# Kernel tuning notes

Hardware: AMD Instinct MI355X
Metric: run time of the kernel (lower is better)

## Reference

```python
import jax, jax.numpy as jnp
import numpy as np

N, E, F_IN, EDGE_DIM, H, C, NUM_RELS = 20000, 160000, 64, 8, 4, 128, 4


def setup_inputs() -> dict:
    key = jax.random.key(0)
    ks = jax.random.split(key, 20)
    def rn(k, shape, s=0.05):
        return jax.random.normal(k, shape, jnp.float32) * s
    return {
        "x": rn(ks[0], (N, F_IN), 1.0),
        "edge_index": jax.random.randint(ks[1], (2, E), 0, N, dtype=jnp.int32),
        "edge_features": rn(ks[2], (E, EDGE_DIM), 1.0),
        "W1": rn(ks[3], (F_IN, H * C)), "a_src1": rn(ks[4], (H, C)), "a_dst1": rn(ks[5], (H, C)),
        "We1": rn(ks[6], (EDGE_DIM, H * C)), "a_e1": rn(ks[7], (H, C)), "b1": jnp.zeros((H * C,), jnp.float32),
        "W2": rn(ks[8], (H * C, H * C)), "a_src2": rn(ks[9], (H, C)), "a_dst2": rn(ks[10], (H, C)),
        "We2": rn(ks[11], (EDGE_DIM, H * C)), "a_e2": rn(ks[12], (H, C)), "b2": jnp.zeros((H * C,), jnp.float32),
        "Wd1": rn(ks[13], (2 * H * C, 256)), "bd1": jnp.zeros((256,), jnp.float32),
        "Wd2": rn(ks[14], (256, NUM_RELS)), "bd2": jnp.zeros((NUM_RELS,), jnp.float32),
    }


def _add_self_loops(ei, ea, n):
    # PyG add_self_loops with fill_value='mean': self-loop edge_attr is the
    # mean of incoming edge_attr per destination node (0 if no incoming edges).
    dst = ei[1]
    s = jax.ops.segment_sum(ea, dst, num_segments=n)
    cnt = jax.ops.segment_sum(jnp.ones((ea.shape[0], 1), ea.dtype), dst, num_segments=n)
    mean = s / jnp.maximum(cnt, 1.0)
    loop = jnp.arange(n, dtype=ei.dtype)
    ei2 = jnp.concatenate([ei, jnp.stack([loop, loop])], axis=1)
    ea2 = jnp.concatenate([ea, mean], axis=0)
    return ei2, ea2


def _gat_conv(x, ei, ea, W, a_s, a_d, We, a_e, b, n):
    ei, ea = _add_self_loops(ei, ea, n)
    src, dst = ei[0], ei[1]
    xp = (x @ W).reshape(n, H, C)                      # [N,H,C]
    alpha_s = jnp.einsum('nhc,hc->nh', xp, a_s)        # [N,H]
    alpha_d = jnp.einsum('nhc,hc->nh', xp, a_d)        # [N,H]
    ep = (ea @ We).reshape(-1, H, C)                   # [E',H,C]
    alpha_e = jnp.einsum('ehc,hc->eh', ep, a_e)        # [E',H]
    alpha = alpha_s[src] + alpha_d[dst] + alpha_e
    alpha = jax.nn.leaky_relu(alpha, 0.2)
    # segment softmax over edges sharing a destination node
    m = jax.ops.segment_max(alpha, dst, num_segments=n)
    ex = jnp.exp(alpha - m[dst])
    den = jax.ops.segment_sum(ex, dst, num_segments=n)
    w = ex / den[dst]                                   # [E',H]
    out = jax.ops.segment_sum(xp[src] * w[..., None], dst, num_segments=n)  # [N,H,C]
    return out.reshape(n, H * C) + b


def reference(x, edge_index, edge_features, W1, a_src1, a_dst1, We1, a_e1, b1,
              W2, a_src2, a_dst2, We2, a_e2, b2, Wd1, bd1, Wd2, bd2):
    n = x.shape[0]
    z = jax.nn.elu(_gat_conv(x, edge_index, edge_features, W1, a_src1, a_dst1, We1, a_e1, b1, n))
    z = jax.nn.elu(_gat_conv(z, edge_index, edge_features, W2, a_src2, a_dst2, We2, a_e2, b2, n))
    src, dst = edge_index[0], edge_index[1]
    rel = jnp.concatenate([z[src], z[dst]], axis=1)     # [E, 2*512]
    h = rel @ Wd1 + bd1                                 # dropout is identity at inference
    return jax.nn.sigmoid(h @ Wd2 + bd2)
```

## Files before the change

kernel.cpp:

```cpp
#include <hip/hip_runtime.h>
#include <hip/hip_bf16.h>
#include <math.h>

#define N_NODES 20000
#define N_EDGES 160000
#define FIN 64
#define EDGE_DIM 8
#define H_HEADS 4
#define C_CH 128
#define HC 512
#define NUM_RELS 4
#define E_TOT (N_EDGES + N_NODES)
#define E_PAD 320256

typedef __bf16 bf16x8 __attribute__((ext_vector_type(8)));
typedef __bf16 bf16x4 __attribute__((ext_vector_type(4)));
typedef float f32x4 __attribute__((ext_vector_type(4)));
typedef unsigned short u16x8 __attribute__((ext_vector_type(8)));

#define NZ4 ((N_NODES + E_PAD) / 4)
#define NM4 (E_PAD / 4)
__global__ void k_fill(int4* __restrict__ zbase, int4* __restrict__ mbase) {
    int tid = blockIdx.x * 256 + threadIdx.x;
    if (tid < NZ4) {
        zbase[tid] = make_int4(0, 0, 0, 0);
    } else if (tid < NZ4 + NM4) {
        mbase[tid - NZ4] = make_int4(-1, -1, -1, -1);
    }
}

#define NX4 (N_NODES * FIN / 4)
#define W1T (HC * FIN)
#define W2T (HC * HC)
#define NCVTB ((NX4 + W1T + W2T) / 256)
__global__ void k_prep_all(const float* __restrict__ x, __bf16* __restrict__ xb,
                           const float* __restrict__ W1, __bf16* __restrict__ Wt1,
                           const float* __restrict__ W2, __bf16* __restrict__ Wt2,
                           const float* __restrict__ We1, const float* __restrict__ ae1,
                           const float* __restrict__ We2, const float* __restrict__ ae2,
                           float* __restrict__ q1, float* __restrict__ q2,
                           const float* __restrict__ Wd1, const float* __restrict__ Wd2,
                           const float* __restrict__ bd1, const float* __restrict__ bd2,
                           float* __restrict__ M, float* __restrict__ cvec,
                           const float* __restrict__ as1, const float* __restrict__ ad1,
                           float* __restrict__ w1as, float* __restrict__ w1ad) {
    int bid = blockIdx.x;
    if (bid < NCVTB) {
        int tid = bid * 256 + threadIdx.x;
        if (tid < NX4) {
            float4 v = *(const float4*)(x + (size_t)tid * 4);
            __bf16 o[4] = {(__bf16)v.x, (__bf16)v.y, (__bf16)v.z, (__bf16)v.w};
            *(ushort2*)(xb + (size_t)tid * 4) = *(ushort2*)o;
            *(ushort2*)(xb + (size_t)tid * 4 + 2) = *(ushort2*)(o + 2);
        } else if (tid < NX4 + W1T) {
            int t = tid - NX4;
            int n = t / FIN, k = t % FIN;
            Wt1[n * FIN + k] = (__bf16)W1[(size_t)k * HC + n];
        } else {
            int t = tid - NX4 - W1T;
            int n = t >> 9, k = t & 511;
            Wt2[n * HC + k] = (__bf16)W2[(size_t)k * HC + n];
        }
        return;
    }
    int pb = bid - NCVTB;
    if (pb == 16) {
        int t = threadIdx.x;
        if (t >= 64) return;
        const float* We = (t < 32) ? We1 : We2;
        const float* ae = (t < 32) ? ae1 : ae2;
        float* q = (t < 32) ? q1 : q2;
        int i = t & 31, h = i >> 3, d = i & 7;
        float s = 0.f;
        for (int c = 0; c < 128; ++c) s += We[d * 512 + h * 128 + c] * ae[h * 128 + c];
        q[i] = s;
    } else if (pb == 17 || pb == 18) {
        int t = threadIdx.x;
        int h = t >> 6, k = t & 63;
        const float* av = (pb == 17) ? as1 : ad1;
        float* outp = (pb == 17) ? w1as : w1ad;
        float s = 0.f;
        for (int c = 0; c < 128; ++c) s += W1[(size_t)k * HC + h * 128 + c] * av[h * 128 + c];
        outp[h * 64 + k] = s;
    } else {
        int tid = pb * 256 + threadIdx.x;
        int i = tid >> 2, r = tid & 3;
        float s = 0.f;
        for (int k = 0; k < 256; ++k) s += Wd1[i * 256 + k] * Wd2[k * 4 + r];
        M[tid] = s;
        if (tid < 4) {
            float c = 0.f;
            for (int k = 0; k < 256; ++k) c += bd1[k] * Wd2[k * 4 + tid];
            cvec[tid] = c + bd2[tid];
        }
    }
}

#define LDP 40
__global__ __launch_bounds__(256)
void k_gemm_bf16(const __bf16* __restrict__ A, const __bf16* __restrict__ Bt,
                 __bf16* __restrict__ Ch, int M, int K) {
    __shared__ __bf16 As[128 * LDP];
    __shared__ __bf16 Bs[128 * LDP];

    int nwg = gridDim.x;
    int f = blockIdx.x;
    int q = nwg >> 3, r = nwg & 7;
    int xcd = f & 7, idx = f >> 3;
    int wg = (xcd < r ? xcd * (q + 1) : r * (q + 1) + (xcd - r) * q) + idx;
    int by = wg >> 2, bx = wg & 3;
    int br = by * 128, bc = bx * 128;

    const int t = threadIdx.x;
    const int lane = t & 63;
    const int wid = t >> 6;
    const int wr = wid >> 1, wc = wid & 1;
    const int l15 = lane & 15, lkg = lane >> 4;

    const int srow = t >> 1, shalf = (t & 1) * 16;
    const int agr = br + srow;
    const __bf16* Ap = A + (size_t)agr * K + shalf;
    const __bf16* Bp = Bt + (size_t)(bc + srow) * K + shalf;

    f32x4 acc[4][4] = {};

    for (int k0 = 0; k0 < K; k0 += 32) {
        u16x8 av0 = {}, av1 = {};
        if (agr < M) {
            av0 = *(const u16x8*)(Ap + k0);
            av1 = *(const u16x8*)(Ap + k0 + 8);
        }
        u16x8 bv0 = *(const u16x8*)(Bp + k0);
        u16x8 bv1 = *(const u16x8*)(Bp + k0 + 8);
        *(u16x8*)(As + srow * LDP + shalf) = av0;
        *(u16x8*)(As + srow * LDP + shalf + 8) = av1;
        *(u16x8*)(Bs + srow * LDP + shalf) = bv0;
        *(u16x8*)(Bs + srow * LDP + shalf + 8) = bv1;
        __syncthreads();

        bf16x8 a[4], b[4];
        #pragma unroll
        for (int m = 0; m < 4; ++m)
            a[m] = *(const bf16x8*)(As + (wr * 64 + m * 16 + l15) * LDP + lkg * 8);
        #pragma unroll
        for (int n = 0; n < 4; ++n)
            b[n] = *(const bf16x8*)(Bs + (wc * 64 + n * 16 + l15) * LDP + lkg * 8);
        #pragma unroll
        for (int m = 0; m < 4; ++m)
            #pragma unroll
            for (int n = 0; n < 4; ++n)
                acc[m][n] = __builtin_amdgcn_mfma_f32_16x16x32_bf16(a[m], b[n], acc[m][n], 0, 0, 0);
        __syncthreads();
    }

    #pragma unroll
    for (int m = 0; m < 4; ++m) {
        int rbase = br + wr * 64 + m * 16 + lkg * 4;
        #pragma unroll
        for (int n = 0; n < 4; ++n) {
            int lcol = wc * 64 + n * 16 + l15;
            #pragma unroll
            for (int rg = 0; rg < 4; ++rg) {
                int gr = rbase + rg;
                if (gr < M)
                    Ch[((size_t)bx * N_NODES + gr) * 128 + lcol] = (__bf16)acc[m][n][rg];
            }
        }
    }
}

__global__ __launch_bounds__(256)
void k_gemm_head(const __bf16* __restrict__ aggb, const __bf16* __restrict__ Wt1,
                 const float* __restrict__ b1, __bf16* __restrict__ z1b, int M) {
    __shared__ __bf16 As[128 * LDP];
    __shared__ __bf16 Bs[128 * LDP];
    const int h = blockIdx.x;
    const int br = blockIdx.y * 128;

    const int t = threadIdx.x;
    const int lane = t & 63;
    const int wid = t >> 6;
    const int wr = wid >> 1, wc = wid & 1;
    const int l15 = lane & 15, lkg = lane >> 4;

    const int srow = t >> 1, shalf = (t & 1) * 16;
    const int agr = br + srow;
    const __bf16* Ap = aggb + (size_t)agr * 256 + h * 64 + shalf;
    const __bf16* Bp = Wt1 + (size_t)(h * 128 + srow) * 64 + shalf;

    f32x4 acc[4][4] = {};

    #pragma unroll
    for (int k0 = 0; k0 < 64; k0 += 32) {
        u16x8 av0 = {}, av1 = {};
        if (agr < M) {
            av0 = *(const u16x8*)(Ap + k0);
            av1 = *(const u16x8*)(Ap + k0 + 8);
        }
        u16x8 bv0 = *(const u16x8*)(Bp + k0);
        u16x8 bv1 = *(const u16x8*)(Bp + k0 + 8);
        *(u16x8*)(As + srow * LDP + shalf) = av0;
        *(u16x8*)(As + srow * LDP + shalf + 8) = av1;
        *(u16x8*)(Bs + srow * LDP + shalf) = bv0;
        *(u16x8*)(Bs + srow * LDP + shalf + 8) = bv1;
        __syncthreads();

        bf16x8 a[4], b[4];
        #pragma unroll
        for (int m = 0; m < 4; ++m)
            a[m] = *(const bf16x8*)(As + (wr * 64 + m * 16 + l15) * LDP + lkg * 8);
        #pragma unroll
        for (int n = 0; n < 4; ++n)
            b[n] = *(const bf16x8*)(Bs + (wc * 64 + n * 16 + l15) * LDP + lkg * 8);
        #pragma unroll
        for (int m = 0; m < 4; ++m)
            #pragma unroll
            for (int n = 0; n < 4; ++n)
                acc[m][n] = __builtin_amdgcn_mfma_f32_16x16x32_bf16(a[m], b[n], acc[m][n], 0, 0, 0);
        __syncthreads();
    }

    #pragma unroll
    for (int m = 0; m < 4; ++m) {
        int rbase = br + wr * 64 + m * 16 + lkg * 4;
        #pragma unroll
        for (int n = 0; n < 4; ++n) {
            int gcol = h * 128 + wc * 64 + n * 16 + l15;
            float bias = b1[gcol];
            #pragma unroll
            for (int rg = 0; rg < 4; ++rg) {
                int gr = rbase + rg;
                if (gr < M) {
                    float v = acc[m][n][rg] + bias;
                    v = (v > 0.f) ? v : expm1f(v);
                    z1b[(size_t)gr * HC + gcol] = (__bf16)v;
                }
            }
        }
    }
}

__global__ void k_count(const int* __restrict__ ei, int* __restrict__ counts) {
    int e = blockIdx.x * 256 + threadIdx.x;
    if (e >= E_TOT) return;
    int dst = (e < N_EDGES) ? ei[N_EDGES + e] : (e - N_EDGES);
    atomicAdd(counts + dst, 1);
}

__global__ __launch_bounds__(1024)
void k_scan(const int* __restrict__ counts, int* __restrict__ row_start,
            int* __restrict__ nxt) {
    __shared__ int part[1024];
    int t = threadIdx.x;
    int base = t * 20;
    int pre[20];
    int s = 0;
    #pragma unroll
    for (int i = 0; i < 20; ++i) {
        int idx = base + i;
        int c = (idx < N_NODES) ? ((counts[idx] + 7) & ~7) : 0;
        pre[i] = s; s += c;
    }
    part[t] = s;
    __syncthreads();
    for (int off = 1; off < 1024; off <<= 1) {
        int v = (t >= off) ? part[t - off] : 0;
        __syncthreads();
        part[t] += v;
        __syncthreads();
    }
    int excl = (t == 0) ? 0 : part[t - 1];
    #pragma unroll
    for (int i = 0; i < 20; ++i) {
        int idx = base + i;
        if (idx < N_NODES) { int v = excl + pre[i]; row_start[idx] = v; nxt[idx] = v; }
    }
    if (t == 1023) row_start[N_NODES] = part[1023];
}

__global__ void k_scatter(const int* __restrict__ ei, int* __restrict__ nxt,
                          int* __restrict__ csr_src, int* __restrict__ csr_eid,
                          int* __restrict__ csr_dst) {
    int e = blockIdx.x * 256 + threadIdx.x;
    if (e >= E_TOT) return;
    int src, dst;
    if (e < N_EDGES) { src = ei[e]; dst = ei[N_EDGES + e]; }
    else             { src = dst = e - N_EDGES; }
    int pos = atomicAdd(nxt + dst, 1);
    csr_src[pos] = src;
    csr_eid[pos] = e;
    csr_dst[pos] = dst;
}

__global__ void k_mean_csr(const int* __restrict__ row_start, const int* __restrict__ csr_eid,
                           const float* __restrict__ ef, float* __restrict__ meanf) {
    int n = blockIdx.x * 32 + (threadIdx.x >> 3);
    int d = threadIdx.x & 7;
    if (n >= N_NODES) return;
    int rs = row_start[n], re = row_start[n + 1];
    float s = 0.f; int c = 0;
    for (int i = rs; i < re; ++i) {
        unsigned eid = (unsigned)csr_eid[i];
        if (eid < N_EDGES) { s += ef[(size_t)eid * 8 + d]; ++c; }
    }
    meanf[n * 8 + d] = s / fmaxf((float)c, 1.f);
}

__global__ __launch_bounds__(256)
void k_nodeab(const __bf16* __restrict__ xb, const float* __restrict__ w1as,
              const float* __restrict__ w1ad, float* __restrict__ as_,
              float* __restrict__ ad_) {
    int n = blockIdx.x * 4 + (threadIdx.x >> 6);
    int lane = threadIdx.x & 63;
    if (n >= N_NODES) return;
    float xv = (float)xb[(size_t)n * 64 + lane];
    float s[4], d[4];
    #pragma unroll
    for (int h = 0; h < 4; ++h) {
        s[h] = xv * w1as[h * 64 + lane];
        d[h] = xv * w1ad[h * 64 + lane];
    }
    #pragma unroll
    for (int off = 32; off; off >>= 1) {
        #pragma unroll
        for (int h = 0; h < 4; ++h) {
            s[h] += __shfl_xor(s[h], off);
            d[h] += __shfl_xor(d[h], off);
        }
    }
    if (lane == 0) {
        *(float4*)(as_ + n * 4) = make_float4(s[0], s[1], s[2], s[3]);
        *(float4*)(ad_ + n * 4) = make_float4(d[0], d[1], d[2], d[3]);
    }
}

__global__ __launch_bounds__(256)
void k_node_alpha_hm(const __bf16* __restrict__ xph, const float* __restrict__ a_s,
                     const float* __restrict__ a_d, float* __restrict__ as_,
                     float* __restrict__ ad_) {
    int n = blockIdx.x * 4 + (threadIdx.x >> 6);
    int lane = threadIdx.x & 63;
    if (n >= N_NODES) return;
    float s[4], d[4];
    #pragma unroll
    for (int h = 0; h < 4; ++h) {
        ushort2 xv = *(const ushort2*)(xph + ((size_t)h * N_NODES + n) * 128 + lane * 2);
        __bf16 b0 = *(const __bf16*)&xv.x, b1v = *(const __bf16*)&xv.y;
        float x0 = (float)b0, x1 = (float)b1v;
        s[h] = x0 * a_s[h * 128 + lane * 2] + x1 * a_s[h * 128 + lane * 2 + 1];
        d[h] = x0 * a_d[h * 128 + lane * 2] + x1 * a_d[h * 128 + lane * 2 + 1];
    }
    #pragma unroll
    for (int off = 32; off; off >>= 1) {
        #pragma unroll
        for (int h = 0; h < 4; ++h) {
            s[h] += __shfl_xor(s[h], off);
            d[h] += __shfl_xor(d[h], off);
        }
    }
    if (lane == 0) {
        *(float4*)(as_ + n * 4) = make_float4(s[0], s[1], s[2], s[3]);
        *(float4*)(ad_ + n * 4) = make_float4(d[0], d[1], d[2], d[3]);
    }
}

__global__ void k_edge_ex(const int* __restrict__ csr_src, const int* __restrict__ csr_dst,
                          const int* __restrict__ csr_eid, const float* __restrict__ ef,
                          const float* __restrict__ meanf, const float* __restrict__ q,
                          const float* __restrict__ as_, const float* __restrict__ ad_,
                          float* __restrict__ wbuf) {
    int i = blockIdx.x * 256 + threadIdx.x;
    if (i >= E_PAD) return;
    int eid = csr_eid[i];
    if (eid == -1) {
        *(float4*)(wbuf + (size_t)i * 4) = make_float4(0.f, 0.f, 0.f, 0.f);
        return;
    }
    int src = csr_src[i], dst = csr_dst[i];
    const float* fe = (eid < N_EDGES) ? (ef + (size_t)eid * 8)
                                      : (meanf + (size_t)(eid - N_EDGES) * 8);
    float f[8];
    #pragma unroll
    for (int d = 0; d < 8; ++d) f[d] = fe[d];
    float4 asv = *(const float4*)(as_ + src * 4);
    float4 adv = *(const float4*)(ad_ + dst * 4);
    const float* asp = &asv.x;
    const float* adp = &adv.x;
    float4 o;
    float* op = &o.x;
    #pragma unroll
    for (int h = 0; h < 4; ++h) {
        float ae = 0.f;
        #pragma unroll
        for (int d = 0; d < 8; ++d) ae += f[d] * q[h * 8 + d];
        float a = asp[h] + adp[h] + ae;
        a = (a > 0.f) ? a : 0.2f * a;
        op[h] = expf(a);
    }
    *(float4*)(wbuf + (size_t)i * 4) = o;
}

__global__ __launch_bounds__(256)
void k_gather1(const int* __restrict__ row_start, const int* __restrict__ csr_src,
               const float* __restrict__ wbuf, const __bf16* __restrict__ xb,
               __bf16* __restrict__ aggb) {
    int wv = threadIdx.x >> 6;
    int n = blockIdx.x * 4 + wv;
    int lane = threadIdx.x & 63;
    if (n >= N_NODES) return;
    int rs = row_start[n], re = row_start[n + 1];
    float acc[4] = {};
    float den[4] = {};

    for (int i = rs; i < re; i += 8) {
        unsigned short xr[8];
        float4 wr[8];
        #pragma unroll
        for (int p = 0; p < 8; ++p) {
            int sp = csr_src[i + p];
            xr[p] = *(const unsigned short*)(xb + (size_t)sp * 64 + lane);
            wr[p] = *(const float4*)(wbuf + (size_t)(i + p) * 4);
        }
        __builtin_amdgcn_sched_barrier(0);
        #pragma unroll
        for (int p = 0; p < 8; ++p) {
            float xv = (float)*(const __bf16*)&xr[p];
            acc[0] += wr[p].x * xv; den[0] += wr[p].x;
            acc[1] += wr[p].y * xv; den[1] += wr[p].y;
            acc[2] += wr[p].z * xv; den[2] += wr[p].z;
            acc[3] += wr[p].w * xv; den[3] += wr[p].w;
        }
    }
    #pragma unroll
    for (int h = 0; h < 4; ++h)
        aggb[(size_t)n * 256 + h * 64 + lane] = (__bf16)(acc[h] / den[h]);
}

__global__ __launch_bounds__(256)
void k_gather2h(const int* __restrict__ row_start, const int* __restrict__ csr_src,
                const float* __restrict__ wbuf, const __bf16* __restrict__ xph,
                const float* __restrict__ b2, __bf16* __restrict__ zh) {
    int h = blockIdx.y;
    int wv = threadIdx.x >> 6;
    int n = blockIdx.x * 4 + wv;
    int lane = threadIdx.x & 63;
    if (n >= N_NODES) return;
    int rs = row_start[n], re = row_start[n + 1];
    const __bf16* xbase = xph + (size_t)h * N_NODES * 128 + lane * 2;
    float a0 = 0.f, a1 = 0.f, den = 0.f;

    int i = rs;
    for (; i + 16 <= re; i += 16) {
        unsigned xr[16];
        float wr[16];
        #pragma unroll
        for (int p = 0; p < 16; ++p) {
            int sp = csr_src[i + p];
            wr[p] = wbuf[(size_t)(i + p) * 4 + h];
            xr[p] = *(const unsigned*)(xbase + (size_t)sp * 128);
        }
        __builtin_amdgcn_sched_barrier(0);
        #pragma unroll
        for (int p = 0; p < 16; ++p) {
            __bf16 b0 = *(const __bf16*)&xr[p];
            __bf16 b1v = *((const __bf16*)&xr[p] + 1);
            den += wr[p];
            a0 += wr[p] * (float)b0;
            a1 += wr[p] * (float)b1v;
        }
    }
    for (; i < re; i += 8) {
        unsigned xr[8];
        float wr[8];
        #pragma unroll
        for (int p = 0; p < 8; ++p) {
            int sp = csr_src[i + p];
            wr[p] = wbuf[(size_t)(i + p) * 4 + h];
            xr[p] = *(const unsigned*)(xbase + (size_t)sp * 128);
        }
        __builtin_amdgcn_sched_barrier(0);
        #pragma unroll
        for (int p = 0; p < 8; ++p) {
            __bf16 b0 = *(const __bf16*)&xr[p];
            __bf16 b1v = *((const __bf16*)&xr[p] + 1);
            den += wr[p];
            a0 += wr[p] * (float)b0;
            a1 += wr[p] * (float)b1v;
        }
    }
    float inv = 1.f / den;
    float v0 = a0 * inv + b2[h * 128 + lane * 2];
    float v1 = a1 * inv + b2[h * 128 + lane * 2 + 1];
    v0 = (v0 > 0.f) ? v0 : expm1f(v0);
    v1 = (v1 > 0.f) ? v1 : expm1f(v1);
    __bf16 o[2] = {(__bf16)v0, (__bf16)v1};
    *(ushort*)(zh + ((size_t)h * N_NODES + n) * 128 + lane * 2) = *(ushort*)&o[0];
    *(ushort*)(zh + ((size_t)h * N_NODES + n) * 128 + lane * 2 + 1) = *(ushort*)&o[1];
}

__global__ __launch_bounds__(256)
void k_uv(const __bf16* __restrict__ zh, const float* __restrict__ Mm,
          float* __restrict__ U, float* __restrict__ V) {
    int n = blockIdx.x * 4 + (threadIdx.x >> 6);
    int lane = threadIdx.x & 63;
    if (n >= N_NODES) return;
    int h = lane >> 4;
    bf16x8 zv = *(const bf16x8*)(zh + ((size_t)h * N_NODES + n) * 128 + (lane & 15) * 8);
    float u[4] = {}, v[4] = {};
    #pragma unroll
    for (int k = 0; k < 8; ++k) {
        float z = (float)zv[k];
        int fidx = lane * 8 + k;
        #pragma unroll
        for (int r = 0; r < 4; ++r) {
            u[r] += z * Mm[fidx * 4 + r];
            v[r] += z * Mm[(512 + fidx) * 4 + r];
        }
    }
    #pragma unroll
    for (int r = 0; r < 4; ++r) {
        #pragma unroll
        for (int off = 32; off; off >>= 1) {
            u[r] += __shfl_xor(u[r], off);
            v[r] += __shfl_xor(v[r], off);
        }
    }
    if (lane == 0) {
        *(float4*)(U + n * 4) = make_float4(u[0], u[1], u[2], u[3]);
        *(float4*)(V + n * 4) = make_float4(v[0], v[1], v[2], v[3]);
    }
}

__global__ void k_edge_out(const int* __restrict__ ei, const float* __restrict__ U,
                           const float* __restrict__ V, const float* __restrict__ cvec,
                           float* __restrict__ out) {
    int e = blockIdx.x * 256 + threadIdx.x;
    if (e >= N_EDGES) return;
    float4 u = *(const float4*)(U + (size_t)ei[e] * 4);
    float4 v = *(const float4*)(V + (size_t)ei[N_EDGES + e] * 4);
    float4 c = *(const float4*)cvec;
    float4 o;
    o.x = 1.f / (1.f + expf(-(u.x + v.x + c.x)));
    o.y = 1.f / (1.f + expf(-(u.y + v.y + c.y)));
    o.z = 1.f / (1.f + expf(-(u.z + v.z + c.z)));
    o.w = 1.f / (1.f + expf(-(u.w + v.w + c.w)));
    *(float4*)(out + (size_t)e * 4) = o;
}

extern "C" void kernel_launch(void* const* d_in, const int* in_sizes, int n_in,
                              void* d_out, int out_size, void* d_ws, size_t ws_size,
                              hipStream_t stream) {
    (void)in_sizes; (void)n_in; (void)out_size; (void)ws_size;
    const float* x      = (const float*)d_in[0];
    const int*   ei     = (const int*)d_in[1];
    const float* ef     = (const float*)d_in[2];
    const float* W1     = (const float*)d_in[3];
    const float* a_src1 = (const float*)d_in[4];
    const float* a_dst1 = (const float*)d_in[5];
    const float* We1    = (const float*)d_in[6];
    const float* a_e1   = (const float*)d_in[7];
    const float* b1     = (const float*)d_in[8];
    const float* W2     = (const float*)d_in[9];
    const float* a_src2 = (const float*)d_in[10];
    const float* a_dst2 = (const float*)d_in[11];
    const float* We2    = (const float*)d_in[12];
    const float* a_e2   = (const float*)d_in[13];
    const float* b2     = (const float*)d_in[14];
    const float* Wd1    = (const float*)d_in[15];
    const float* bd1    = (const float*)d_in[16];
    const float* Wd2    = (const float*)d_in[17];
    const float* bd2    = (const float*)d_in[18];
    float* out = (float*)d_out;

    float* wbuf   = (float*)d_ws;
    float* as_    = wbuf + (size_t)E_PAD * 4;
    float* ad_    = as_ + N_NODES * 4;
    float* meanf  = ad_ + N_NODES * 4;
    float* q1     = meanf + N_NODES * 8;
    float* q2     = q1 + 32;
    float* w1as   = q2 + 32;
    float* w1ad   = w1as + 256;
    float* Mm     = w1ad + 256;
    float* cv     = Mm + 4096;
    float* U      = cv + 4;
    float* V      = U + N_NODES * 4;
    int* row_start = (int*)(V + N_NODES * 4);
    int* nxt       = row_start + 20004;
    int* counts    = nxt + N_NODES;
    int* csr_src   = counts + N_NODES;
    int* csr_eid   = csr_src + E_PAD;
    int* csr_dst   = csr_eid + E_PAD;
    __bf16* xb   = (__bf16*)(csr_dst + E_PAD);
    __bf16* aggb = xb + (size_t)N_NODES * FIN;
    __bf16* z1b  = aggb + (size_t)N_NODES * 256;
    __bf16* xph2 = z1b + (size_t)N_NODES * HC;
    __bf16* Wt1  = xph2 + (size_t)N_NODES * HC;
    __bf16* Wt2  = Wt1 + HC * FIN;
    __bf16* zh   = z1b;

    k_fill<<<(NZ4 + NM4 + 255) / 256, 256, 0, stream>>>((int4*)counts, (int4*)csr_eid);
    k_count<<<(E_TOT + 255) / 256, 256, 0, stream>>>(ei, counts);
    k_scan<<<1, 1024, 0, stream>>>(counts, row_start, nxt);
    k_scatter<<<(E_TOT + 255) / 256, 256, 0, stream>>>(ei, nxt, csr_src, csr_eid, csr_dst);
    k_mean_csr<<<(N_NODES + 31) / 32, 256, 0, stream>>>(row_start, csr_eid, ef, meanf);
    k_prep_all<<<NCVTB + 19, 256, 0, stream>>>(x, xb, W1, Wt1, W2, Wt2,
                                               We1, a_e1, We2, a_e2, q1, q2,
                                               Wd1, Wd2, bd1, bd2, Mm, cv,
                                               a_src1, a_dst1, w1as, w1ad);

    const int nblk = (N_NODES + 3) / 4;
    const int nby = (N_NODES + 127) / 128;

    k_nodeab<<<nblk, 256, 0, stream>>>(xb, w1as, w1ad, as_, ad_);
    k_edge_ex<<<(E_PAD + 255) / 256, 256, 0, stream>>>(csr_src, csr_dst, csr_eid, ef, meanf,
                                                       q1, as_, ad_, wbuf);
    k_gather1<<<nblk, 256, 0, stream>>>(row_start, csr_src, wbuf, xb, aggb);
    k_gemm_head<<<dim3(4, nby), 256, 0, stream>>>(aggb, Wt1, b1, z1b, N_NODES);

    k_gemm_bf16<<<nby * 4, 256, 0, stream>>>(z1b, Wt2, xph2, N_NODES, HC);
    k_node_alpha_hm<<<nblk, 256, 0, stream>>>(xph2, a_src2, a_dst2, as_, ad_);
    k_edge_ex<<<(E_PAD + 255) / 256, 256, 0, stream>>>(csr_src, csr_dst, csr_eid, ef, meanf,
                                                       q2, as_, ad_, wbuf);
    k_gather2h<<<dim3(nblk, 4), 256, 0, stream>>>(row_start, csr_src, wbuf, xph2, b2, zh);
    k_uv<<<nblk, 256, 0, stream>>>(zh, Mm, U, V);

    k_edge_out<<<(N_EDGES + 255) / 256, 256, 0, stream>>>(ei, U, V, cv, out);
}
```

Baseline: 264.5 us.

## Fuse layer-2 attention logits into GEMM epilogue and U/V projection into gather

Computes the layer-2 per-node source/destination attention logits inside the GEMM epilogue using shuffle and shared-memory reductions, which removes the separate k_node_alpha_hm pass over xph2. It also folds the decoder's low-rank projection into k_gather2h, which now writes per-head partial U/V vectors instead of the bf16 z tensor, so k_uv and the z round-trip go away. In exchange, k_edge_out now gathers four partial float4s per endpoint instead of one, and the GEMM epilogue takes on extra reductions and a barrier.

```diff
diff --git a/kernel.cpp b/kernel.cpp
--- a/kernel.cpp
+++ b/kernel.cpp
@@ -99,7 +99,9 @@
 #define LDP 40
 __global__ __launch_bounds__(256)
 void k_gemm_bf16(const __bf16* __restrict__ A, const __bf16* __restrict__ Bt,
-                 __bf16* __restrict__ Ch, int M, int K) {
+                 __bf16* __restrict__ Ch, int M, int K,
+                 const float* __restrict__ a_s2, const float* __restrict__ a_d2,
+                 float* __restrict__ as_, float* __restrict__ ad_) {
     __shared__ __bf16 As[128 * LDP];
     __shared__ __bf16 Bs[128 * LDP];
 
@@ -165,6 +167,46 @@
                 if (gr < M)
                     Ch[((size_t)bx * N_NODES + gr) * 128 + lcol] = (__bf16)acc[m][n][rg];
             }
+        }
+    }
+
+    float as_w[4], ad_w[4];
+    #pragma unroll
+    for (int n = 0; n < 4; ++n) {
+        int col = wc * 64 + n * 16 + l15;
+        as_w[n] = a_s2[bx * 128 + col];
+        ad_w[n] = a_d2[bx * 128 + col];
+    }
+    float* sred = (float*)As;
+    #pragma unroll
+    for (int m = 0; m < 4; ++m) {
+        #pragma unroll
+        for (int rg = 0; rg < 4; ++rg) {
+            float s = 0.f, d = 0.f;
+            #pragma unroll
+            for (int n = 0; n < 4; ++n) {
+                float c = acc[m][n][rg];
+                s += c * as_w[n];
+                d += c * ad_w[n];
+            }
+            #pragma unroll
+            for (int off = 1; off <= 8; off <<= 1) {
+                s += __shfl_xor(s, off);
+                d += __shfl_xor(d, off);
+            }
+            if (l15 == 0) {
+                int lrow = wr * 64 + m * 16 + lkg * 4 + rg;
+                sred[lrow * 2 + wc] = s;
+                sred[256 + lrow * 2 + wc] = d;
+            }
+        }
+    }
+    __syncthreads();
+    if (t < 128) {
+        int gr = br + t;
+        if (gr < M) {
+            as_[gr * 4 + bx] = sred[t * 2] + sred[t * 2 + 1];
+            ad_[gr * 4 + bx] = sred[256 + t * 2] + sred[256 + t * 2 + 1];
         }
     }
 }
@@ -334,36 +376,6 @@
     }
 }
 
-__global__ __launch_bounds__(256)
-void k_node_alpha_hm(const __bf16* __restrict__ xph, const float* __restrict__ a_s,
-                     const float* __restrict__ a_d, float* __restrict__ as_,
-                     float* __restrict__ ad_) {
-    int n = blockIdx.x * 4 + (threadIdx.x >> 6);
-    int lane = threadIdx.x & 63;
-    if (n >= N_NODES) return;
-    float s[4], d[4];
-    #pragma unroll
-    for (int h = 0; h < 4; ++h) {
-        ushort2 xv = *(const ushort2*)(xph + ((size_t)h * N_NODES + n) * 128 + lane * 2);
-        __bf16 b0 = *(const __bf16*)&xv.x, b1v = *(const __bf16*)&xv.y;
-        float x0 = (float)b0, x1 = (float)b1v;
-        s[h] = x0 * a_s[h * 128 + lane * 2] + x1 * a_s[h * 128 + lane * 2 + 1];
-        d[h] = x0 * a_d[h * 128 + lane * 2] + x1 * a_d[h * 128 + lane * 2 + 1];
-    }
-    #pragma unroll
-    for (int off = 32; off; off >>= 1) {
-        #pragma unroll
-        for (int h = 0; h < 4; ++h) {
-            s[h] += __shfl_xor(s[h], off);
-            d[h] += __shfl_xor(d[h], off);
-        }
-    }
-    if (lane == 0) {
-        *(float4*)(as_ + n * 4) = make_float4(s[0], s[1], s[2], s[3]);
-        *(float4*)(ad_ + n * 4) = make_float4(d[0], d[1], d[2], d[3]);
-    }
-}
-
 __global__ void k_edge_ex(const int* __restrict__ csr_src, const int* __restrict__ csr_dst,
                           const int* __restrict__ csr_eid, const float* __restrict__ ef,
                           const float* __restrict__ meanf, const float* __restrict__ q,
@@ -439,7 +451,8 @@
 __global__ __launch_bounds__(256)
 void k_gather2h(const int* __restrict__ row_start, const int* __restrict__ csr_src,
                 const float* __restrict__ wbuf, const __bf16* __restrict__ xph,
-                const float* __restrict__ b2, __bf16* __restrict__ zh) {
+                const float* __restrict__ b2, const float* __restrict__ Mm,
+                float* __restrict__ Up, float* __restrict__ Vp) {
     int h = blockIdx.y;
     int wv = threadIdx.x >> 6;
     int n = blockIdx.x * 4 + wv;
@@ -493,51 +506,44 @@
     float v1 = a1 * inv + b2[h * 128 + lane * 2 + 1];
     v0 = (v0 > 0.f) ? v0 : expm1f(v0);
     v1 = (v1 > 0.f) ? v1 : expm1f(v1);
-    __bf16 o[2] = {(__bf16)v0, (__bf16)v1};
-    *(ushort*)(zh + ((size_t)h * N_NODES + n) * 128 + lane * 2) = *(ushort*)&o[0];
-    *(ushort*)(zh + ((size_t)h * N_NODES + n) * 128 + lane * 2 + 1) = *(ushort*)&o[1];
-}
-
-__global__ __launch_bounds__(256)
-void k_uv(const __bf16* __restrict__ zh, const float* __restrict__ Mm,
-          float* __restrict__ U, float* __restrict__ V) {
-    int n = blockIdx.x * 4 + (threadIdx.x >> 6);
-    int lane = threadIdx.x & 63;
-    if (n >= N_NODES) return;
-    int h = lane >> 4;
-    bf16x8 zv = *(const bf16x8*)(zh + ((size_t)h * N_NODES + n) * 128 + (lane & 15) * 8);
-    float u[4] = {}, v[4] = {};
-    #pragma unroll
-    for (int k = 0; k < 8; ++k) {
-        float z = (float)zv[k];
-        int fidx = lane * 8 + k;
+
+    const float* m0 = Mm + (h * 128 + lane * 2) * 4;
+    const float* n0 = Mm + 2048 + (h * 128 + lane * 2) * 4;
+    float up[4], vp[4];
+    #pragma unroll
+    for (int r = 0; r < 4; ++r) {
+        up[r] = v0 * m0[r] + v1 * m0[4 + r];
+        vp[r] = v0 * n0[r] + v1 * n0[4 + r];
+    }
+    #pragma unroll
+    for (int off = 32; off; off >>= 1) {
         #pragma unroll
         for (int r = 0; r < 4; ++r) {
-            u[r] += z * Mm[fidx * 4 + r];
-            v[r] += z * Mm[(512 + fidx) * 4 + r];
-        }
-    }
-    #pragma unroll
-    for (int r = 0; r < 4; ++r) {
-        #pragma unroll
-        for (int off = 32; off; off >>= 1) {
-            u[r] += __shfl_xor(u[r], off);
-            v[r] += __shfl_xor(v[r], off);
+            up[r] += __shfl_xor(up[r], off);
+            vp[r] += __shfl_xor(vp[r], off);
         }
     }
     if (lane == 0) {
-        *(float4*)(U + n * 4) = make_float4(u[0], u[1], u[2], u[3]);
-        *(float4*)(V + n * 4) = make_float4(v[0], v[1], v[2], v[3]);
-    }
-}
-
-__global__ void k_edge_out(const int* __restrict__ ei, const float* __restrict__ U,
-                           const float* __restrict__ V, const float* __restrict__ cvec,
+        *(float4*)(Up + ((size_t)h * N_NODES + n) * 4) = make_float4(up[0], up[1], up[2], up[3]);
+        *(float4*)(Vp + ((size_t)h * N_NODES + n) * 4) = make_float4(vp[0], vp[1], vp[2], vp[3]);
+    }
+}
+
+__global__ void k_edge_out(const int* __restrict__ ei, const float* __restrict__ Up,
+                           const float* __restrict__ Vp, const float* __restrict__ cvec,
                            float* __restrict__ out) {
     int e = blockIdx.x * 256 + threadIdx.x;
     if (e >= N_EDGES) return;
-    float4 u = *(const float4*)(U + (size_t)ei[e] * 4);
-    float4 v = *(const float4*)(V + (size_t)ei[N_EDGES + e] * 4);
+    int s = ei[e], d = ei[N_EDGES + e];
+    float4 u = make_float4(0.f, 0.f, 0.f, 0.f);
+    float4 v = make_float4(0.f, 0.f, 0.f, 0.f);
+    #pragma unroll
+    for (int h = 0; h < 4; ++h) {
+        float4 uh = *(const float4*)(Up + ((size_t)h * N_NODES + s) * 4);
+        float4 vh = *(const float4*)(Vp + ((size_t)h * N_NODES + d) * 4);
+        u.x += uh.x; u.y += uh.y; u.z += uh.z; u.w += uh.w;
+        v.x += vh.x; v.y += vh.y; v.z += vh.z; v.w += vh.w;
+    }
     float4 c = *(const float4*)cvec;
     float4 o;
     o.x = 1.f / (1.f + expf(-(u.x + v.x + c.x)));
@@ -582,9 +588,9 @@
     float* w1ad   = w1as + 256;
     float* Mm     = w1ad + 256;
     float* cv     = Mm + 4096;
-    float* U      = cv + 4;
-    float* V      = U + N_NODES * 4;
-    int* row_start = (int*)(V + N_NODES * 4);
+    float* Up     = cv + 4;
+    float* Vp     = Up + (size_t)N_NODES * 16;
+    int* row_start = (int*)(Vp + (size_t)N_NODES * 16);
     int* nxt       = row_start + 20004;
     int* counts    = nxt + N_NODES;
     int* csr_src   = counts + N_NODES;
@@ -596,7 +602,6 @@
     __bf16* xph2 = z1b + (size_t)N_NODES * HC;
     __bf16* Wt1  = xph2 + (size_t)N_NODES * HC;
     __bf16* Wt2  = Wt1 + HC * FIN;
-    __bf16* zh   = z1b;
 
     k_fill<<<(NZ4 + NM4 + 255) / 256, 256, 0, stream>>>((int4*)counts, (int4*)csr_eid);
     k_count<<<(E_TOT + 255) / 256, 256, 0, stream>>>(ei, counts);
@@ -617,12 +622,12 @@
     k_gather1<<<nblk, 256, 0, stream>>>(row_start, csr_src, wbuf, xb, aggb);
     k_gemm_head<<<dim3(4, nby), 256, 0, stream>>>(aggb, Wt1, b1, z1b, N_NODES);
 
-    k_gemm_bf16<<<nby * 4, 256, 0, stream>>>(z1b, Wt2, xph2, N_NODES, HC);
-    k_node_alpha_hm<<<nblk, 256, 0, stream>>>(xph2, a_src2, a_dst2, as_, ad_);
+    k_gemm_bf16<<<nby * 4, 256, 0, stream>>>(z1b, Wt2, xph2, N_NODES, HC,
+                                             a_src2, a_dst2, as_, ad_);
     k_edge_ex<<<(E_PAD + 255) / 256, 256, 0, stream>>>(csr_src, csr_dst, csr_eid, ef, meanf,
                                                        q2, as_, ad_, wbuf);
-    k_gather2h<<<dim3(nblk, 4), 256, 0, stream>>>(row_start, csr_src, wbuf, xph2, b2, zh);
-    k_uv<<<nblk, 256, 0, stream>>>(zh, Mm, U, V);
-
-    k_edge_out<<<(N_EDGES + 255) / 256, 256, 0, stream>>>(ei, U, V, cv, out);
-}
+    k_gather2h<<<dim3(nblk, 4), 256, 0, stream>>>(row_start, csr_src, wbuf, xph2, b2,
+                                                  Mm, Up, Vp);
+
+    k_edge_out<<<(N_EDGES + 255) / 256, 256, 0, stream>>>(ei, Up, Vp, cv, out);
+}
```

Result: faster. 235.1 us (-11.1%).
